# Optimization experiments

Hardware: AMD Instinct MI355X
Metric: run time of the kernel (lower is better)

## Reference

```python
import jax, jax.numpy as jnp
import numpy as np

NHEAD = 16
HEAD_DIM = 64
EMBED_DIM = NHEAD * HEAD_DIM  # 1024
U, R, L, M = 2048, 256, 1024, 512


def setup_inputs() -> dict:
    key = jax.random.key(0)
    ks = jax.random.split(key, 11)
    D = EMBED_DIM
    inp = {
        "utterance": jax.random.normal(ks[0], (U, 1, D), jnp.float32),
        "right_context": jax.random.normal(ks[1], (R, 1, D), jnp.float32),
        "memory": jax.random.normal(ks[2], (M, 1, D), jnp.float32),
        "left_context_key": jax.random.normal(ks[3], (L, 1, D), jnp.float32),
        "left_context_val": jax.random.normal(ks[4], (L, 1, D), jnp.float32),
        "Wq": jax.random.normal(ks[5], (D, D), jnp.float32) * 0.02,
        "bq": jax.random.normal(ks[6], (D,), jnp.float32) * 0.02,
        "Wkv": jax.random.normal(ks[7], (2 * D, D), jnp.float32) * 0.02,
        "bkv": jax.random.normal(ks[8], (2 * D,), jnp.float32) * 0.02,
        "Wo": jax.random.normal(ks[9], (D, D), jnp.float32) * 0.02,
        "bo": jax.random.normal(ks[10], (D,), jnp.float32) * 0.02,
    }
    return inp


def reference(utterance, right_context, memory, left_context_key, left_context_val,
              Wq, bq, Wkv, bkv, Wo, bo):
    D = EMBED_DIM
    scaling = HEAD_DIM ** (-0.5)

    # query = Linear([right_context; utterance])  -> (Q, 1, D), Q = R + U
    q_in = jnp.concatenate([right_context, utterance], axis=0)
    query = q_in @ Wq.T + bq

    # key/value = Linear([memory; right_context; utterance]) split in two
    kv_in = jnp.concatenate([memory, right_context, utterance], axis=0)
    kv = kv_in @ Wkv.T + bkv  # (M+R+U, 1, 2D)
    k_new, v_new = kv[..., :D], kv[..., D:]

    # insert cached left-context key/value after [memory; right_context]
    key = jnp.concatenate([k_new[: M + R], left_context_key, k_new[M + R:]], axis=0)
    value = jnp.concatenate([v_new[: M + R], left_context_val, v_new[M + R:]], axis=0)

    Q = U + R
    KV = M + R + L + U
    # (T, 1, D) -> (nhead, T, head_dim)
    q = query.reshape(Q, NHEAD, HEAD_DIM).transpose(1, 0, 2)
    k = key.reshape(KV, NHEAD, HEAD_DIM).transpose(1, 0, 2)
    v = value.reshape(KV, NHEAD, HEAD_DIM).transpose(1, 0, 2)

    weights = jnp.einsum("hqd,hkd->hqk", q * scaling, k)  # (nhead, Q, KV)
    probs = jax.nn.softmax(weights, axis=-1)
    attn = jnp.einsum("hqk,hkd->hqd", probs, v)  # (nhead, Q, head_dim)

    attn = attn.transpose(1, 0, 2).reshape(Q, D)[:, None, :]  # (Q, 1, D)
    out = attn @ Wo.T + bo
    return out, key, value
```

## Files before the change

### kernel.cpp

```cpp
#include <hip/hip_runtime.h>
#include <hip/hip_bf16.h>

#define EMBED   1024
#define NHEADS  16
#define HDIM    64
#define U_LEN   2048
#define R_LEN   256
#define L_LEN   1024
#define M_LEN   512
#define Q_LEN   (U_LEN + R_LEN)
#define KV_LEN  (M_LEN + R_LEN + L_LEN + U_LEN)
#define X_ROWS  (M_LEN + R_LEN + U_LEN)
#define NPART   6
#define KV_PART (KV_LEN / NPART)

typedef __attribute__((ext_vector_type(8))) short short8;
typedef __attribute__((ext_vector_type(4))) float f32x4;
typedef __attribute__((ext_vector_type(16))) float f32x16;

#define QSCALE 0.180336880f

__device__ __forceinline__ void gl2lds16(const __hip_bfloat16* g, __hip_bfloat16* l) {
  __builtin_amdgcn_global_load_lds(
      (const __attribute__((address_space(1))) unsigned int*)g,
      (__attribute__((address_space(3))) unsigned int*)l, 16, 0, 0);
}

__device__ __forceinline__ unsigned pack_bf16(float a, float b) {
  unsigned ua = __builtin_bit_cast(unsigned, a) + 0x8000u;
  unsigned ub = __builtin_bit_cast(unsigned, b) + 0x8000u;
  return (ua >> 16) | (ub & 0xFFFF0000u);
}

__global__ __launch_bounds__(256) void prep_kernel(
    const float* __restrict__ mem, const float* __restrict__ rc,
    const float* __restrict__ utt, const float* __restrict__ lk,
    const float* __restrict__ lv, const float* __restrict__ Wq,
    const float* __restrict__ Wkv, const float* __restrict__ Wo,
    __hip_bfloat16* __restrict__ X, __hip_bfloat16* __restrict__ WB,
    __hip_bfloat16* __restrict__ WoB,
    float* __restrict__ key_out, float* __restrict__ val_out,
    __hip_bfloat16* __restrict__ k_bf, __hip_bfloat16* __restrict__ v_bf) {
  int b = blockIdx.x, tid = threadIdx.x;
  if (b < 2816) {
    int row = b, col = tid * 4;
    const float* src;
    if (row < M_LEN)              src = mem + row * EMBED;
    else if (row < M_LEN + R_LEN) src = rc + (row - M_LEN) * EMBED;
    else                          src = utt + (row - M_LEN - R_LEN) * EMBED;
    float4 v = *reinterpret_cast<const float4*>(src + col);
    __hip_bfloat16* d = X + (size_t)row * EMBED + col;
    d[0] = __float2bfloat16(v.x); d[1] = __float2bfloat16(v.y);
    d[2] = __float2bfloat16(v.z); d[3] = __float2bfloat16(v.w);
  } else if (b < 6912) {
    const float* src; __hip_bfloat16* dst;
    int blk;
    if (b < 3840)      { src = Wq;  dst = WB;                blk = b - 2816; }
    else if (b < 5888) { src = Wkv; dst = WB + 1024 * 1024;  blk = b - 3840; }
    else               { src = Wo;  dst = WoB;               blk = b - 5888; }
    int idx = blk * 1024 + tid * 4;
    float4 v = *reinterpret_cast<const float4*>(src + idx);
    dst[idx + 0] = __float2bfloat16(v.x);
    dst[idx + 1] = __float2bfloat16(v.y);
    dst[idx + 2] = __float2bfloat16(v.z);
    dst[idx + 3] = __float2bfloat16(v.w);
  } else {
    int row = b - 6912, c0 = tid * 4;
    int orow = 768 + row;
    float4 kv4 = *reinterpret_cast<const float4*>(lk + row * EMBED + c0);
    float4 vv4 = *reinterpret_cast<const float4*>(lv + row * EMBED + c0);
    *reinterpret_cast<float4*>(key_out + (size_t)orow * EMBED + c0) = kv4;
    *reinterpret_cast<float4*>(val_out + (size_t)orow * EMBED + c0) = vv4;
    __hip_bfloat16* kd = k_bf + (size_t)orow * EMBED + c0;
    __hip_bfloat16* vd = v_bf + (size_t)orow * EMBED + c0;
    kd[0] = __float2bfloat16(kv4.x); kd[1] = __float2bfloat16(kv4.y);
    kd[2] = __float2bfloat16(kv4.z); kd[3] = __float2bfloat16(kv4.w);
    vd[0] = __float2bfloat16(vv4.x); vd[1] = __float2bfloat16(vv4.y);
    vd[2] = __float2bfloat16(vv4.z); vd[3] = __float2bfloat16(vv4.w);
  }
}

__global__ __launch_bounds__(256) void transpose_kernel(
    const unsigned short* __restrict__ v_bf, unsigned short* __restrict__ vT) {
  __shared__ unsigned short T[64][72];
  int kt = blockIdx.x * 64, d0 = blockIdx.y * 64;
  int t = threadIdx.x;
  int r = t >> 3, c = (t & 7) * 8;
#pragma unroll
  for (int half = 0; half < 2; half++) {
    int kv = r + half * 32;
    short8 v = *reinterpret_cast<const short8*>(v_bf + (size_t)(kt + kv) * EMBED + d0 + c);
#pragma unroll
    for (int j = 0; j < 8; j++) T[c + j][kv] = (unsigned short)v[j];
  }
  __syncthreads();
#pragma unroll
  for (int half = 0; half < 2; half++) {
    int d = r + half * 32;
    *reinterpret_cast<short8*>(vT + (size_t)(d0 + d) * KV_LEN + kt + c) =
        *reinterpret_cast<const short8*>(&T[d][c]);
  }
}

__global__ __launch_bounds__(256) void gemm_qkv(
    const __hip_bfloat16* __restrict__ A, const __hip_bfloat16* __restrict__ B,
    const float* __restrict__ bq, const float* __restrict__ bkv,
    float* __restrict__ key_out, float* __restrict__ val_out,
    __hip_bfloat16* __restrict__ q_bf, __hip_bfloat16* __restrict__ k_bf,
    __hip_bfloat16* __restrict__ v_bf) {
  __shared__ __align__(16) __hip_bfloat16 As[128 * 32];
  __shared__ __align__(16) __hip_bfloat16 Bs[128 * 32];
  const int K = EMBED;
  int tid = threadIdx.x;
  int wave = tid >> 6, lane = tid & 63, quad = lane >> 4, l16 = lane & 15;
  int wm = wave >> 1, wn = wave & 1;
  int mbase = blockIdx.y * 128, nbase = blockIdx.x * 128;

  if (nbase < 1024 && mbase + 128 <= 512) return;

  const __hip_bfloat16* a0 = A + (size_t)(mbase + (tid >> 2)) * K + (tid & 3) * 8;
  const __hip_bfloat16* a1 = a0 + (size_t)64 * K;
  const __hip_bfloat16* b0 = B + (size_t)(nbase + (tid >> 2)) * K + (tid & 3) * 8;
  const __hip_bfloat16* b1 = b0 + (size_t)64 * K;
  __hip_bfloat16* lA0 = As + tid * 8;
  __hip_bfloat16* lA1 = As + (tid + 256) * 8;
  __hip_bfloat16* lB0 = Bs + tid * 8;
  __hip_bfloat16* lB1 = Bs + (tid + 256) * 8;

  f32x4 acc[4][4] = {};
  for (int kt = 0; kt < K; kt += 32) {
    gl2lds16(a0 + kt, lA0);
    gl2lds16(a1 + kt, lA1);
    gl2lds16(b0 + kt, lB0);
    gl2lds16(b1 + kt, lB1);
    __syncthreads();
    short8 af[4], bfr[4];
#pragma unroll
    for (int i = 0; i < 4; i++)
      af[i] = *reinterpret_cast<const short8*>(As + (wm * 64 + i * 16 + l16) * 32 + quad * 8);
#pragma unroll
    for (int j = 0; j < 4; j++)
      bfr[j] = *reinterpret_cast<const short8*>(Bs + (wn * 64 + j * 16 + l16) * 32 + quad * 8);
#pragma unroll
    for (int i = 0; i < 4; i++)
#pragma unroll
      for (int j = 0; j < 4; j++)
        acc[i][j] = __builtin_amdgcn_mfma_f32_16x16x32_bf16(af[i], bfr[j], acc[i][j], 0, 0, 0);
    __syncthreads();
  }

#pragma unroll
  for (int i = 0; i < 4; i++) {
    int rb = mbase + wm * 64 + i * 16 + quad * 4;
#pragma unroll
    for (int j = 0; j < 4; j++) {
      int cg = nbase + wn * 64 + j * 16 + l16;
      float bv = (cg < 1024) ? bq[cg] : bkv[cg - 1024];
#pragma unroll
      for (int reg = 0; reg < 4; reg++) {
        int rg = rb + reg;
        float val = acc[i][j][reg] + bv;
        if (cg < 1024) {
          if (rg >= 512)
            q_bf[(size_t)(rg - 512) * 1024 + cg] = __float2bfloat16(val * QSCALE);
        } else {
          int orow = (rg < 768) ? rg : rg + 1024;
          if (cg < 2048) {
            int cc = cg - 1024;
            key_out[(size_t)orow * 1024 + cc] = val;
            k_bf[(size_t)orow * 1024 + cc] = __float2bfloat16(val);
          } else {
            int cc = cg - 2048;
            val_out[(size_t)orow * 1024 + cc] = val;
            v_bf[(size_t)orow * 1024 + cc] = __float2bfloat16(val);
          }
        }
      }
    }
  }
}

__global__ __launch_bounds__(256) void gemm_out(
    const __hip_bfloat16* __restrict__ A, const __hip_bfloat16* __restrict__ B,
    const float* __restrict__ bias, float* __restrict__ outf) {
  __shared__ __align__(16) __hip_bfloat16 As[64 * 32];
  __shared__ __align__(16) __hip_bfloat16 Bs[128 * 32];
  const int K = EMBED, N = EMBED;
  int tid = threadIdx.x;
  int wave = tid >> 6, lane = tid & 63, quad = lane >> 4, l16 = lane & 15;
  int wm = wave >> 1, wn = wave & 1;
  int mbase = blockIdx.y * 64, nbase = blockIdx.x * 128;

  const __hip_bfloat16* a0 = A + (size_t)(mbase + (tid >> 2)) * K + (tid & 3) * 8;
  const __hip_bfloat16* b0 = B + (size_t)(nbase + (tid >> 2)) * K + (tid & 3) * 8;
  const __hip_bfloat16* b1 = b0 + (size_t)64 * K;
  __hip_bfloat16* lA0 = As + tid * 8;
  __hip_bfloat16* lB0 = Bs + tid * 8;
  __hip_bfloat16* lB1 = Bs + (tid + 256) * 8;

  f32x4 acc[2][4] = {};
  for (int kt = 0; kt < K; kt += 32) {
    gl2lds16(a0 + kt, lA0);
    gl2lds16(b0 + kt, lB0);
    gl2lds16(b1 + kt, lB1);
    __syncthreads();
    short8 af[2], bfr[4];
#pragma unroll
    for (int i = 0; i < 2; i++)
      af[i] = *reinterpret_cast<const short8*>(As + (wm * 32 + i * 16 + l16) * 32 + quad * 8);
#pragma unroll
    for (int j = 0; j < 4; j++)
      bfr[j] = *reinterpret_cast<const short8*>(Bs + (wn * 64 + j * 16 + l16) * 32 + quad * 8);
#pragma unroll
    for (int i = 0; i < 2; i++)
#pragma unroll
      for (int j = 0; j < 4; j++)
        acc[i][j] = __builtin_amdgcn_mfma_f32_16x16x32_bf16(af[i], bfr[j], acc[i][j], 0, 0, 0);
    __syncthreads();
  }

#pragma unroll
  for (int i = 0; i < 2; i++) {
    int rb = mbase + wm * 32 + i * 16 + quad * 4;
#pragma unroll
    for (int j = 0; j < 4; j++) {
      int cg = nbase + wn * 64 + j * 16 + l16;
      float bv = bias[cg];
#pragma unroll
      for (int reg = 0; reg < 4; reg++)
        outf[(size_t)(rb + reg) * N + cg] = acc[i][j][reg] + bv;
    }
  }
}

__global__ __launch_bounds__(256, 4) void attn_kernel(
    const __hip_bfloat16* __restrict__ q_bf, const __hip_bfloat16* __restrict__ k_bf,
    const __hip_bfloat16* __restrict__ vT,
    __hip_bfloat16* __restrict__ o_part, float* __restrict__ lsum) {
  __shared__ __align__(16) __hip_bfloat16 Ks[64][72];
  __shared__ __align__(16) __hip_bfloat16 VTs[64][72];
  int tid = threadIdx.x;
  int w = tid >> 6, lane = tid & 63, l31 = lane & 31, h2 = lane >> 5;
  int h = blockIdx.y, part = blockIdx.z;
  int qbase = blockIdx.x * 128;
  int qg = qbase + w * 32 + l31;

  short8 Qf[4];
#pragma unroll
  for (int ks = 0; ks < 4; ks++)
    Qf[ks] = *reinterpret_cast<const short8*>(
        q_bf + (size_t)qg * EMBED + h * HDIM + ks * 16 + h2 * 8);

  f32x16 ot[2] = {};
  float l_run = 0.f;

  int sr = tid >> 3, sc = (tid & 7) * 8;
  const int kv0 = part * KV_PART;

  for (int kt = kv0; kt < kv0 + KV_PART; kt += 64) {
#pragma unroll
    for (int half = 0; half < 2; half++) {
      int r = sr + half * 32;
      *reinterpret_cast<short8*>(&Ks[r][sc]) =
          *reinterpret_cast<const short8*>(k_bf + (size_t)(kt + r) * EMBED + h * HDIM + sc);
      *reinterpret_cast<short8*>(&VTs[r][sc]) =
          *reinterpret_cast<const short8*>(vT + (size_t)(h * HDIM + r) * KV_LEN + kt + sc);
    }
    __syncthreads();

#pragma unroll
    for (int kvs = 0; kvs < 2; kvs++) {
      f32x16 s = {};
#pragma unroll
      for (int ks = 0; ks < 4; ks++) {
        short8 ak = *reinterpret_cast<const short8*>(&Ks[kvs * 32 + l31][ks * 16 + h2 * 8]);
        s = __builtin_amdgcn_mfma_f32_32x32x16_bf16(ak, Qf[ks], s, 0, 0, 0);
      }
      unsigned u[4][2];
#pragma unroll
      for (int g = 0; g < 4; g++) {
        float p0 = exp2f(s[4 * g + 0]), p1 = exp2f(s[4 * g + 1]);
        float p2 = exp2f(s[4 * g + 2]), p3 = exp2f(s[4 * g + 3]);
        l_run += (p0 + p1) + (p2 + p3);
        u[g][0] = pack_bf16(p0, p1);
        u[g][1] = pack_bf16(p2, p3);
      }
#pragma unroll
      for (int half = 0; half < 2; half++) {
        int c = kvs * 2 + half;
        int gA = 2 * half, gB = 2 * half + 1;
        unsigned s0 = h2 ? u[gA][0] : u[gB][0];
        unsigned s1 = h2 ? u[gA][1] : u[gB][1];
        unsigned r0 = __shfl_xor(s0, 32, 64);
        unsigned r1 = __shfl_xor(s1, 32, 64);
        uint4 fr;
        fr.x = h2 ? r0 : u[gA][0];
        fr.y = h2 ? r1 : u[gA][1];
        fr.z = h2 ? u[gB][0] : r0;
        fr.w = h2 ? u[gB][1] : r1;
        short8 pf = __builtin_bit_cast(short8, fr);
#pragma unroll
        for (int ds = 0; ds < 2; ds++) {
          short8 av = *reinterpret_cast<const short8*>(&VTs[ds * 32 + l31][c * 16 + h2 * 8]);
          ot[ds] = __builtin_amdgcn_mfma_f32_32x32x16_bf16(av, pf, ot[ds], 0, 0, 0);
        }
      }
    }
    __syncthreads();
  }

  l_run += __shfl_xor(l_run, 32, 64);
  float inv = 1.0f / l_run;

  size_t orow = (size_t)part * Q_LEN + qg;
#pragma unroll
  for (int ds = 0; ds < 2; ds++)
#pragma unroll
    for (int g = 0; g < 4; g++) {
      uint2 pk;
      pk.x = pack_bf16(ot[ds][4 * g + 0] * inv, ot[ds][4 * g + 1] * inv);
      pk.y = pack_bf16(ot[ds][4 * g + 2] * inv, ot[ds][4 * g + 3] * inv);
      *reinterpret_cast<uint2*>(
          o_part + orow * 1024 + h * HDIM + ds * 32 + g * 8 + h2 * 4) = pk;
    }
  if (lane < 32)
    lsum[orow * NHEADS + h] = l_run;
}

__global__ __launch_bounds__(256) void merge_kernel(
    const __hip_bfloat16* __restrict__ o_part, const float* __restrict__ lsum,
    __hip_bfloat16* __restrict__ attn_bf) {
  int q = blockIdx.x;
  int c = threadIdx.x * 4;
  int h = c >> 6;
  float wt[NPART], L = 0.f;
#pragma unroll
  for (int p = 0; p < NPART; p++) {
    wt[p] = lsum[((size_t)p * Q_LEN + q) * NHEADS + h];
    L += wt[p];
  }
  float invL = 1.0f / L;
  float acc[4] = {0.f, 0.f, 0.f, 0.f};
#pragma unroll
  for (int p = 0; p < NPART; p++) {
    __hip_bfloat16 v[4];
    *reinterpret_cast<uint2*>(v) =
        *reinterpret_cast<const uint2*>(o_part + ((size_t)p * Q_LEN + q) * 1024 + c);
#pragma unroll
    for (int j = 0; j < 4; j++) acc[j] += wt[p] * __bfloat162float(v[j]);
  }
  uint2 pk;
  pk.x = pack_bf16(acc[0] * invL, acc[1] * invL);
  pk.y = pack_bf16(acc[2] * invL, acc[3] * invL);
  *reinterpret_cast<uint2*>(attn_bf + (size_t)q * 1024 + c) = pk;
}


extern "C" void kernel_launch(void* const* d_in, const int* in_sizes, int n_in,
                              void* d_out, int out_size, void* d_ws, size_t ws_size,
                              hipStream_t stream) {
  const float* utt = (const float*)d_in[0];
  const float* rc  = (const float*)d_in[1];
  const float* mem = (const float*)d_in[2];
  const float* lk  = (const float*)d_in[3];
  const float* lv  = (const float*)d_in[4];
  const float* Wq  = (const float*)d_in[5];
  const float* bq  = (const float*)d_in[6];
  const float* Wkv = (const float*)d_in[7];
  const float* bkv = (const float*)d_in[8];
  const float* Wo  = (const float*)d_in[9];
  const float* bo  = (const float*)d_in[10];

  float* out_f   = (float*)d_out;
  float* key_out = out_f + Q_LEN * EMBED;
  float* val_out = key_out + KV_LEN * EMBED;

  char* ws = (char*)d_ws;
  size_t off = 0;
  __hip_bfloat16* X_bf   = (__hip_bfloat16*)(ws + off); off += (size_t)X_ROWS * EMBED * 2;
  __hip_bfloat16* WB_bf  = (__hip_bfloat16*)(ws + off); off += (size_t)3 * EMBED * EMBED * 2;
  __hip_bfloat16* Wo_bf  = (__hip_bfloat16*)(ws + off); off += (size_t)EMBED * EMBED * 2;
  __hip_bfloat16* q_bf   = (__hip_bfloat16*)(ws + off); off += (size_t)Q_LEN * EMBED * 2;
  __hip_bfloat16* k_bf   = (__hip_bfloat16*)(ws + off); off += (size_t)KV_LEN * EMBED * 2;
  __hip_bfloat16* vT_bf  = (__hip_bfloat16*)(ws + off); off += (size_t)EMBED * KV_LEN * 2;
  __hip_bfloat16* o_part = (__hip_bfloat16*)(ws + off); off += (size_t)NPART * Q_LEN * EMBED * 2;
  __hip_bfloat16* attn_bf = X_bf;
  float* lsum = (float*)WB_bf;
  __hip_bfloat16* v_bf = o_part;
  (void)off; (void)ws_size; (void)in_sizes; (void)n_in; (void)out_size;

  prep_kernel<<<7936, 256, 0, stream>>>(mem, rc, utt, lk, lv, Wq, Wkv, Wo,
                                        X_bf, WB_bf, Wo_bf,
                                        key_out, val_out, k_bf, v_bf);
  gemm_qkv<<<dim3(3 * EMBED / 128, X_ROWS / 128), 256, 0, stream>>>(
      X_bf, WB_bf, bq, bkv, key_out, val_out, q_bf, k_bf, v_bf);
  transpose_kernel<<<dim3(KV_LEN / 64, EMBED / 64), 256, 0, stream>>>(
      (const unsigned short*)v_bf, (unsigned short*)vT_bf);
  attn_kernel<<<dim3(Q_LEN / 128, NHEADS, NPART), 256, 0, stream>>>(
      q_bf, k_bf, vT_bf, o_part, lsum);
  merge_kernel<<<Q_LEN, 256, 0, stream>>>(o_part, lsum, attn_bf);
  gemm_out<<<dim3(EMBED / 128, Q_LEN / 64), 256, 0, stream>>>(
      attn_bf, Wo_bf, bo, out_f);
}
```

Baseline: 243.0 us.

## Retile QKV GEMM, split-K output GEMM, and process two query tiles per attention wave

The QKV projection GEMM now uses 128x64 tiles instead of 128x128, doubling the grid for better CU occupancy. The output projection becomes split-K over two halves with 64x64 tiles, writing fp32 partials that a new reduce kernel sums and adds the bias to. The attention kernel has each wave handle 64 queries, two 32-row groups, so every K and V LDS fragment is reused across both groups. Its launch bound drops to 3 blocks per CU to allow more registers. The cost is an extra kernel launch plus partial-sum traffic, and higher register pressure in attention.

```diff
diff --git a/kernel.cpp b/kernel.cpp
--- a/kernel.cpp
+++ b/kernel.cpp
@@ -109,42 +109,39 @@
     __hip_bfloat16* __restrict__ q_bf, __hip_bfloat16* __restrict__ k_bf,
     __hip_bfloat16* __restrict__ v_bf) {
   __shared__ __align__(16) __hip_bfloat16 As[128 * 32];
-  __shared__ __align__(16) __hip_bfloat16 Bs[128 * 32];
+  __shared__ __align__(16) __hip_bfloat16 Bs[64 * 32];
   const int K = EMBED;
   int tid = threadIdx.x;
   int wave = tid >> 6, lane = tid & 63, quad = lane >> 4, l16 = lane & 15;
   int wm = wave >> 1, wn = wave & 1;
-  int mbase = blockIdx.y * 128, nbase = blockIdx.x * 128;
+  int mbase = blockIdx.y * 128, nbase = blockIdx.x * 64;
 
   if (nbase < 1024 && mbase + 128 <= 512) return;
 
   const __hip_bfloat16* a0 = A + (size_t)(mbase + (tid >> 2)) * K + (tid & 3) * 8;
   const __hip_bfloat16* a1 = a0 + (size_t)64 * K;
   const __hip_bfloat16* b0 = B + (size_t)(nbase + (tid >> 2)) * K + (tid & 3) * 8;
-  const __hip_bfloat16* b1 = b0 + (size_t)64 * K;
   __hip_bfloat16* lA0 = As + tid * 8;
   __hip_bfloat16* lA1 = As + (tid + 256) * 8;
   __hip_bfloat16* lB0 = Bs + tid * 8;
-  __hip_bfloat16* lB1 = Bs + (tid + 256) * 8;
-
-  f32x4 acc[4][4] = {};
+
+  f32x4 acc[4][2] = {};
   for (int kt = 0; kt < K; kt += 32) {
     gl2lds16(a0 + kt, lA0);
     gl2lds16(a1 + kt, lA1);
     gl2lds16(b0 + kt, lB0);
-    gl2lds16(b1 + kt, lB1);
-    __syncthreads();
-    short8 af[4], bfr[4];
+    __syncthreads();
+    short8 af[4], bfr[2];
 #pragma unroll
     for (int i = 0; i < 4; i++)
       af[i] = *reinterpret_cast<const short8*>(As + (wm * 64 + i * 16 + l16) * 32 + quad * 8);
 #pragma unroll
-    for (int j = 0; j < 4; j++)
-      bfr[j] = *reinterpret_cast<const short8*>(Bs + (wn * 64 + j * 16 + l16) * 32 + quad * 8);
+    for (int j = 0; j < 2; j++)
+      bfr[j] = *reinterpret_cast<const short8*>(Bs + (wn * 32 + j * 16 + l16) * 32 + quad * 8);
 #pragma unroll
     for (int i = 0; i < 4; i++)
 #pragma unroll
-      for (int j = 0; j < 4; j++)
+      for (int j = 0; j < 2; j++)
         acc[i][j] = __builtin_amdgcn_mfma_f32_16x16x32_bf16(af[i], bfr[j], acc[i][j], 0, 0, 0);
     __syncthreads();
   }
@@ -153,8 +150,8 @@
   for (int i = 0; i < 4; i++) {
     int rb = mbase + wm * 64 + i * 16 + quad * 4;
 #pragma unroll
-    for (int j = 0; j < 4; j++) {
-      int cg = nbase + wn * 64 + j * 16 + l16;
+    for (int j = 0; j < 2; j++) {
+      int cg = nbase + wn * 32 + j * 16 + l16;
       float bv = (cg < 1024) ? bq[cg] : bkv[cg - 1024];
 #pragma unroll
       for (int reg = 0; reg < 4; reg++) {
@@ -182,39 +179,38 @@
 
 __global__ __launch_bounds__(256) void gemm_out(
     const __hip_bfloat16* __restrict__ A, const __hip_bfloat16* __restrict__ B,
-    const float* __restrict__ bias, float* __restrict__ outf) {
+    float* __restrict__ partial) {
   __shared__ __align__(16) __hip_bfloat16 As[64 * 32];
-  __shared__ __align__(16) __hip_bfloat16 Bs[128 * 32];
+  __shared__ __align__(16) __hip_bfloat16 Bs[64 * 32];
   const int K = EMBED, N = EMBED;
   int tid = threadIdx.x;
   int wave = tid >> 6, lane = tid & 63, quad = lane >> 4, l16 = lane & 15;
   int wm = wave >> 1, wn = wave & 1;
-  int mbase = blockIdx.y * 64, nbase = blockIdx.x * 128;
-
-  const __hip_bfloat16* a0 = A + (size_t)(mbase + (tid >> 2)) * K + (tid & 3) * 8;
-  const __hip_bfloat16* b0 = B + (size_t)(nbase + (tid >> 2)) * K + (tid & 3) * 8;
-  const __hip_bfloat16* b1 = b0 + (size_t)64 * K;
+  int mbase = blockIdx.y * 64, nbase = blockIdx.x * 64;
+  int kbase = blockIdx.z * 512;
+  float* outp = partial + (size_t)blockIdx.z * Q_LEN * EMBED;
+
+  const __hip_bfloat16* a0 = A + (size_t)(mbase + (tid >> 2)) * K + kbase + (tid & 3) * 8;
+  const __hip_bfloat16* b0 = B + (size_t)(nbase + (tid >> 2)) * K + kbase + (tid & 3) * 8;
   __hip_bfloat16* lA0 = As + tid * 8;
   __hip_bfloat16* lB0 = Bs + tid * 8;
-  __hip_bfloat16* lB1 = Bs + (tid + 256) * 8;
-
-  f32x4 acc[2][4] = {};
-  for (int kt = 0; kt < K; kt += 32) {
+
+  f32x4 acc[2][2] = {};
+  for (int kt = 0; kt < 512; kt += 32) {
     gl2lds16(a0 + kt, lA0);
     gl2lds16(b0 + kt, lB0);
-    gl2lds16(b1 + kt, lB1);
-    __syncthreads();
-    short8 af[2], bfr[4];
+    __syncthreads();
+    short8 af[2], bfr[2];
 #pragma unroll
     for (int i = 0; i < 2; i++)
       af[i] = *reinterpret_cast<const short8*>(As + (wm * 32 + i * 16 + l16) * 32 + quad * 8);
 #pragma unroll
-    for (int j = 0; j < 4; j++)
-      bfr[j] = *reinterpret_cast<const short8*>(Bs + (wn * 64 + j * 16 + l16) * 32 + quad * 8);
+    for (int j = 0; j < 2; j++)
+      bfr[j] = *reinterpret_cast<const short8*>(Bs + (wn * 32 + j * 16 + l16) * 32 + quad * 8);
 #pragma unroll
     for (int i = 0; i < 2; i++)
 #pragma unroll
-      for (int j = 0; j < 4; j++)
+      for (int j = 0; j < 2; j++)
         acc[i][j] = __builtin_amdgcn_mfma_f32_16x16x32_bf16(af[i], bfr[j], acc[i][j], 0, 0, 0);
     __syncthreads();
   }
@@ -223,17 +219,29 @@
   for (int i = 0; i < 2; i++) {
     int rb = mbase + wm * 32 + i * 16 + quad * 4;
 #pragma unroll
-    for (int j = 0; j < 4; j++) {
-      int cg = nbase + wn * 64 + j * 16 + l16;
-      float bv = bias[cg];
+    for (int j = 0; j < 2; j++) {
+      int cg = nbase + wn * 32 + j * 16 + l16;
 #pragma unroll
       for (int reg = 0; reg < 4; reg++)
-        outf[(size_t)(rb + reg) * N + cg] = acc[i][j][reg] + bv;
+        outp[(size_t)(rb + reg) * N + cg] = acc[i][j][reg];
     }
   }
 }
 
-__global__ __launch_bounds__(256, 4) void attn_kernel(
+__global__ __launch_bounds__(256) void reduce_out_kernel(
+    const float* __restrict__ partial, const float* __restrict__ bias,
+    float* __restrict__ outf) {
+  int row = blockIdx.x, c = threadIdx.x * 4;
+  float4 p0 = *reinterpret_cast<const float4*>(partial + (size_t)row * EMBED + c);
+  float4 p1 = *reinterpret_cast<const float4*>(partial + (size_t)(Q_LEN + row) * EMBED + c);
+  float4 bv = *reinterpret_cast<const float4*>(bias + c);
+  float4 o;
+  o.x = p0.x + p1.x + bv.x; o.y = p0.y + p1.y + bv.y;
+  o.z = p0.z + p1.z + bv.z; o.w = p0.w + p1.w + bv.w;
+  *reinterpret_cast<float4*>(outf + (size_t)row * EMBED + c) = o;
+}
+
+__global__ __launch_bounds__(256, 3) void attn_kernel(
     const __hip_bfloat16* __restrict__ q_bf, const __hip_bfloat16* __restrict__ k_bf,
     const __hip_bfloat16* __restrict__ vT,
     __hip_bfloat16* __restrict__ o_part, float* __restrict__ lsum) {
@@ -242,17 +250,19 @@
   int tid = threadIdx.x;
   int w = tid >> 6, lane = tid & 63, l31 = lane & 31, h2 = lane >> 5;
   int h = blockIdx.y, part = blockIdx.z;
-  int qbase = blockIdx.x * 128;
-  int qg = qbase + w * 32 + l31;
-
-  short8 Qf[4];
-#pragma unroll
-  for (int ks = 0; ks < 4; ks++)
-    Qf[ks] = *reinterpret_cast<const short8*>(
-        q_bf + (size_t)qg * EMBED + h * HDIM + ks * 16 + h2 * 8);
-
-  f32x16 ot[2] = {};
-  float l_run = 0.f;
+  int qbase = blockIdx.x * 256;
+
+  short8 Qf[2][4];
+#pragma unroll
+  for (int qs = 0; qs < 2; qs++)
+#pragma unroll
+    for (int ks = 0; ks < 4; ks++)
+      Qf[qs][ks] = *reinterpret_cast<const short8*>(
+          q_bf + (size_t)(qbase + w * 64 + qs * 32 + l31) * EMBED +
+          h * HDIM + ks * 16 + h2 * 8);
+
+  f32x16 ot[2][2] = {};
+  float l_run[2] = {0.f, 0.f};
 
   int sr = tid >> 3, sc = (tid & 7) * 8;
   const int kv0 = part * KV_PART;
@@ -270,61 +280,72 @@
 
 #pragma unroll
     for (int kvs = 0; kvs < 2; kvs++) {
-      f32x16 s = {};
-#pragma unroll
-      for (int ks = 0; ks < 4; ks++) {
-        short8 ak = *reinterpret_cast<const short8*>(&Ks[kvs * 32 + l31][ks * 16 + h2 * 8]);
-        s = __builtin_amdgcn_mfma_f32_32x32x16_bf16(ak, Qf[ks], s, 0, 0, 0);
+      short8 ak[4];
+#pragma unroll
+      for (int ks = 0; ks < 4; ks++)
+        ak[ks] = *reinterpret_cast<const short8*>(&Ks[kvs * 32 + l31][ks * 16 + h2 * 8]);
+
+      unsigned u[2][4][2];
+#pragma unroll
+      for (int qs = 0; qs < 2; qs++) {
+        f32x16 s = {};
+#pragma unroll
+        for (int ks = 0; ks < 4; ks++)
+          s = __builtin_amdgcn_mfma_f32_32x32x16_bf16(ak[ks], Qf[qs][ks], s, 0, 0, 0);
+#pragma unroll
+        for (int g = 0; g < 4; g++) {
+          float p0 = exp2f(s[4 * g + 0]), p1 = exp2f(s[4 * g + 1]);
+          float p2 = exp2f(s[4 * g + 2]), p3 = exp2f(s[4 * g + 3]);
+          l_run[qs] += (p0 + p1) + (p2 + p3);
+          u[qs][g][0] = pack_bf16(p0, p1);
+          u[qs][g][1] = pack_bf16(p2, p3);
+        }
       }
-      unsigned u[4][2];
-#pragma unroll
-      for (int g = 0; g < 4; g++) {
-        float p0 = exp2f(s[4 * g + 0]), p1 = exp2f(s[4 * g + 1]);
-        float p2 = exp2f(s[4 * g + 2]), p3 = exp2f(s[4 * g + 3]);
-        l_run += (p0 + p1) + (p2 + p3);
-        u[g][0] = pack_bf16(p0, p1);
-        u[g][1] = pack_bf16(p2, p3);
-      }
+
 #pragma unroll
       for (int half = 0; half < 2; half++) {
         int c = kvs * 2 + half;
         int gA = 2 * half, gB = 2 * half + 1;
-        unsigned s0 = h2 ? u[gA][0] : u[gB][0];
-        unsigned s1 = h2 ? u[gA][1] : u[gB][1];
-        unsigned r0 = __shfl_xor(s0, 32, 64);
-        unsigned r1 = __shfl_xor(s1, 32, 64);
-        uint4 fr;
-        fr.x = h2 ? r0 : u[gA][0];
-        fr.y = h2 ? r1 : u[gA][1];
-        fr.z = h2 ? u[gB][0] : r0;
-        fr.w = h2 ? u[gB][1] : r1;
-        short8 pf = __builtin_bit_cast(short8, fr);
-#pragma unroll
-        for (int ds = 0; ds < 2; ds++) {
-          short8 av = *reinterpret_cast<const short8*>(&VTs[ds * 32 + l31][c * 16 + h2 * 8]);
-          ot[ds] = __builtin_amdgcn_mfma_f32_32x32x16_bf16(av, pf, ot[ds], 0, 0, 0);
+        short8 av0 = *reinterpret_cast<const short8*>(&VTs[l31][c * 16 + h2 * 8]);
+        short8 av1 = *reinterpret_cast<const short8*>(&VTs[32 + l31][c * 16 + h2 * 8]);
+#pragma unroll
+        for (int qs = 0; qs < 2; qs++) {
+          unsigned s0 = h2 ? u[qs][gA][0] : u[qs][gB][0];
+          unsigned s1 = h2 ? u[qs][gA][1] : u[qs][gB][1];
+          unsigned r0 = __shfl_xor(s0, 32, 64);
+          unsigned r1 = __shfl_xor(s1, 32, 64);
+          uint4 fr;
+          fr.x = h2 ? r0 : u[qs][gA][0];
+          fr.y = h2 ? r1 : u[qs][gA][1];
+          fr.z = h2 ? u[qs][gB][0] : r0;
+          fr.w = h2 ? u[qs][gB][1] : r1;
+          short8 pf = __builtin_bit_cast(short8, fr);
+          ot[qs][0] = __builtin_amdgcn_mfma_f32_32x32x16_bf16(av0, pf, ot[qs][0], 0, 0, 0);
+          ot[qs][1] = __builtin_amdgcn_mfma_f32_32x32x16_bf16(av1, pf, ot[qs][1], 0, 0, 0);
         }
       }
     }
     __syncthreads();
   }
 
-  l_run += __shfl_xor(l_run, 32, 64);
-  float inv = 1.0f / l_run;
-
-  size_t orow = (size_t)part * Q_LEN + qg;
-#pragma unroll
-  for (int ds = 0; ds < 2; ds++)
-#pragma unroll
-    for (int g = 0; g < 4; g++) {
-      uint2 pk;
-      pk.x = pack_bf16(ot[ds][4 * g + 0] * inv, ot[ds][4 * g + 1] * inv);
-      pk.y = pack_bf16(ot[ds][4 * g + 2] * inv, ot[ds][4 * g + 3] * inv);
-      *reinterpret_cast<uint2*>(
-          o_part + orow * 1024 + h * HDIM + ds * 32 + g * 8 + h2 * 4) = pk;
-    }
-  if (lane < 32)
-    lsum[orow * NHEADS + h] = l_run;
+#pragma unroll
+  for (int qs = 0; qs < 2; qs++) {
+    l_run[qs] += __shfl_xor(l_run[qs], 32, 64);
+    float inv = 1.0f / l_run[qs];
+    size_t orow = (size_t)part * Q_LEN + qbase + w * 64 + qs * 32 + l31;
+#pragma unroll
+    for (int ds = 0; ds < 2; ds++)
+#pragma unroll
+      for (int g = 0; g < 4; g++) {
+        uint2 pk;
+        pk.x = pack_bf16(ot[qs][ds][4 * g + 0] * inv, ot[qs][ds][4 * g + 1] * inv);
+        pk.y = pack_bf16(ot[qs][ds][4 * g + 2] * inv, ot[qs][ds][4 * g + 3] * inv);
+        *reinterpret_cast<uint2*>(
+            o_part + orow * 1024 + h * HDIM + ds * 32 + g * 8 + h2 * 4) = pk;
+      }
+    if (lane < 32)
+      lsum[orow * NHEADS + h] = l_run[qs];
+  }
 }
 
 __global__ __launch_bounds__(256) void merge_kernel(
@@ -387,18 +408,20 @@
   __hip_bfloat16* attn_bf = X_bf;
   float* lsum = (float*)WB_bf;
   __hip_bfloat16* v_bf = o_part;
+  float* out_partial = (float*)q_bf;
   (void)off; (void)ws_size; (void)in_sizes; (void)n_in; (void)out_size;
 
   prep_kernel<<<7936, 256, 0, stream>>>(mem, rc, utt, lk, lv, Wq, Wkv, Wo,
                                         X_bf, WB_bf, Wo_bf,
                                         key_out, val_out, k_bf, v_bf);
-  gemm_qkv<<<dim3(3 * EMBED / 128, X_ROWS / 128), 256, 0, stream>>>(
+  gemm_qkv<<<dim3(3 * EMBED / 64, X_ROWS / 128), 256, 0, stream>>>(
       X_bf, WB_bf, bq, bkv, key_out, val_out, q_bf, k_bf, v_bf);
   transpose_kernel<<<dim3(KV_LEN / 64, EMBED / 64), 256, 0, stream>>>(
       (const unsigned short*)v_bf, (unsigned short*)vT_bf);
-  attn_kernel<<<dim3(Q_LEN / 128, NHEADS, NPART), 256, 0, stream>>>(
+  attn_kernel<<<dim3(Q_LEN / 256, NHEADS, NPART), 256, 0, stream>>>(
       q_bf, k_bf, vT_bf, o_part, lsum);
   merge_kernel<<<Q_LEN, 256, 0, stream>>>(o_part, lsum, attn_bf);
-  gemm_out<<<dim3(EMBED / 128, Q_LEN / 64), 256, 0, stream>>>(
-      attn_bf, Wo_bf, bo, out_f);
-}
+  gemm_out<<<dim3(EMBED / 64, Q_LEN / 64, 2), 256, 0, stream>>>(
+      attn_bf, Wo_bf, out_partial);
+  reduce_out_kernel<<<Q_LEN, 256, 0, stream>>>(out_partial, bo, out_f);
+}
```

Result: slower. 296.1 us (+21.8%).
